# Performance work log

Measured on AMD Instinct MI355X. Metric: run time of the kernel, lower is better.

The kernel has to match this reference:

```python
import jax, jax.numpy as jnp
import numpy as np

N, M, D_MODEL, H, D_K, D_V = 2048, 2048, 1024, 16, 64, 64


def setup_inputs() -> dict:
    key = jax.random.key(0)
    ks = jax.random.split(key, 12)
    s = D_MODEL ** -0.5
    Q = jax.random.normal(ks[0], (N, D_MODEL), dtype=jnp.float32)
    K = jax.random.normal(ks[1], (M, D_MODEL), dtype=jnp.float32)
    V = jax.random.normal(ks[2], (M, D_MODEL), dtype=jnp.float32)
    mask = jnp.ones((N, M), dtype=bool)  # unused by the original forward
    # stacked per-head Linear params (torch Linear: y = x @ W.T + b); here stored as (H, in, out)
    Wq = jax.random.normal(ks[3], (H, D_MODEL, D_K), dtype=jnp.float32) * s
    bq = jax.random.normal(ks[4], (H, D_K), dtype=jnp.float32) * 0.01
    Wk = jax.random.normal(ks[5], (H, D_MODEL, D_K), dtype=jnp.float32) * s
    bk = jax.random.normal(ks[6], (H, D_K), dtype=jnp.float32) * 0.01
    Wv = jax.random.normal(ks[7], (H, D_MODEL, D_V), dtype=jnp.float32) * s
    bv = jax.random.normal(ks[8], (H, D_V), dtype=jnp.float32) * 0.01
    Wo = jax.random.normal(ks[9], (H * D_V, D_MODEL), dtype=jnp.float32) * ((H * D_V) ** -0.5)
    bo = jax.random.normal(ks[10], (D_MODEL,), dtype=jnp.float32) * 0.01
    return dict(Q=Q, K=K, V=V, mask=mask, Wq=Wq, bq=bq, Wk=Wk, bk=bk,
                Wv=Wv, bv=bv, Wo=Wo, bo=bo)


def reference(Q, K, V, mask, Wq, bq, Wk, bk, Wv, bv, Wo, bo):
    # per-head projections, batched over heads (h)
    Qh = jnp.einsum('nd,hdk->hnk', Q, Wq) + bq[:, None, :]  # (H, n, d_k)
    Kh = jnp.einsum('md,hdk->hmk', K, Wk) + bk[:, None, :]  # (H, m, d_k)
    Vh = jnp.einsum('md,hdv->hmv', V, Wv) + bv[:, None, :]  # (H, m, d_v)
    # faithful to source: scale d_k**-0.5 is applied AFTER the softmax
    scores = jnp.einsum('hnk,hmk->hnm', Qh, Kh)             # (H, n, m)
    attn = jax.nn.softmax(scores, axis=-1) * (D_K ** -0.5)
    heads = jnp.einsum('hnm,hmv->hnv', attn, Vh)            # (H, n, d_v)
    concat = jnp.transpose(heads, (1, 0, 2)).reshape(heads.shape[1], H * D_V)
    return concat @ Wo + bo                                  # (n, d_model)
```

## Files before the change

### kernel.cpp

```cpp
#include <hip/hip_runtime.h>

#define N_TOK 2048
#define DMODEL 1024
#define NH 16
#define DK 64
#define SOFF 48.0f

typedef __attribute__((ext_vector_type(8))) short bfrag;
typedef __attribute__((ext_vector_type(4))) float f32x4;
typedef __attribute__((ext_vector_type(16))) float f32x16;
typedef __attribute__((ext_vector_type(4))) unsigned u32x4;

__device__ __forceinline__ unsigned short f2bf(float f) {
    unsigned u = __builtin_bit_cast(unsigned, f);
    u += 0x7FFFu + ((u >> 16) & 1u);
    return (unsigned short)(u >> 16);
}
__device__ __forceinline__ float bf2f(unsigned short u) {
    unsigned x = ((unsigned)u) << 16;
    return __builtin_bit_cast(float, x);
}
__device__ __forceinline__ unsigned cvtpk(float lo, float hi) {
    unsigned r;
    asm volatile("v_cvt_pk_bf16_f32 %0, %1, %2" : "=v"(r) : "v"(lo), "v"(hi));
    return r;
}

__device__ __forceinline__ int swz(int row, int b) {
    return row * 128 + (b ^ ((row & 7) << 4));
}

__device__ __forceinline__ void gload16(const void* g, void* l) {
    __builtin_amdgcn_global_load_lds(
        (__attribute__((address_space(1))) void*)g,
        (__attribute__((address_space(3))) void*)l,
        16, 0, 0);
}

__global__ __launch_bounds__(256) void prep_kernel(
    const float* __restrict__ Qin, const float* __restrict__ Kin, const float* __restrict__ Vin,
    const float* __restrict__ Wq_, const float* __restrict__ Wk_, const float* __restrict__ Wv_,
    const float* __restrict__ Wo_,
    unsigned short* __restrict__ AhQ, unsigned short* __restrict__ AhK, unsigned short* __restrict__ AhV,
    unsigned short* __restrict__ WthQ, unsigned short* __restrict__ WthK, unsigned short* __restrict__ WthV,
    unsigned short* __restrict__ WoT)
{
    const int bid = blockIdx.x;
    const int tid = threadIdx.x;
    __shared__ float lds[64][65];

    if (bid < 3072) {
        const int z = bid >> 10, x = bid & 1023;
        const float* src = (z == 0) ? Qin : (z == 1) ? Kin : Vin;
        unsigned short* dh = (z == 0) ? AhQ : (z == 1) ? AhK : AhV;
        size_t base = ((size_t)x * 256 + tid) * 8;
        float4 a = *reinterpret_cast<const float4*>(src + base);
        float4 b = *reinterpret_cast<const float4*>(src + base + 4);
        float f[8] = {a.x, a.y, a.z, a.w, b.x, b.y, b.z, b.w};
        unsigned short hb[8];
        #pragma unroll
        for (int i = 0; i < 8; ++i) hb[i] = f2bf(f[i]);
        *reinterpret_cast<uint4*>(dh + base) = *reinterpret_cast<const uint4*>(hb);
    } else if (bid < 3840) {
        const int t = bid - 3072;
        const int z = t >> 8, rem = t & 255;
        const int h = rem >> 4, dt = rem & 15;
        const float* W = (z == 0) ? Wq_ : (z == 1) ? Wk_ : Wv_;
        unsigned short* oh = (z == 0) ? WthQ : (z == 1) ? WthK : WthV;

        {
            int rr = tid >> 2, c4 = (tid & 3) * 16;
            const float* src = W + ((size_t)h * DMODEL + dt * 64 + rr) * DK + c4;
            #pragma unroll
            for (int i = 0; i < 4; ++i) {
                float4 v = *reinterpret_cast<const float4*>(src + i * 4);
                lds[rr][c4 + i * 4 + 0] = v.x;
                lds[rr][c4 + i * 4 + 1] = v.y;
                lds[rr][c4 + i * 4 + 2] = v.z;
                lds[rr][c4 + i * 4 + 3] = v.w;
            }
        }
        __syncthreads();
        {
            int kk_ = tid >> 2, d4 = (tid & 3) * 16;
            unsigned short hb[16];
            #pragma unroll
            for (int i = 0; i < 16; ++i) hb[i] = f2bf(lds[d4 + i][kk_]);
            size_t o = (size_t)(h * 64 + kk_) * DMODEL + dt * 64 + d4;
            *reinterpret_cast<uint4*>(oh + o)     = *reinterpret_cast<const uint4*>(hb);
            *reinterpret_cast<uint4*>(oh + o + 8) = *reinterpret_cast<const uint4*>(hb + 8);
        }
    } else {
        const int t = bid - 3840;
        const int dt = t >> 4, jt = t & 15;
        {
            int rr = tid >> 2, c4 = (tid & 3) * 16;
            const float* src = Wo_ + (size_t)(dt * 64 + rr) * DMODEL + jt * 64 + c4;
            #pragma unroll
            for (int i = 0; i < 4; ++i) {
                float4 v = *reinterpret_cast<const float4*>(src + i * 4);
                lds[rr][c4 + i * 4 + 0] = v.x;
                lds[rr][c4 + i * 4 + 1] = v.y;
                lds[rr][c4 + i * 4 + 2] = v.z;
                lds[rr][c4 + i * 4 + 3] = v.w;
            }
        }
        __syncthreads();
        {
            int jj = tid >> 2, d4 = (tid & 3) * 16;
            unsigned short hb[16];
            #pragma unroll
            for (int i = 0; i < 16; ++i) hb[i] = f2bf(lds[d4 + i][jj]);
            size_t o = (size_t)(jt * 64 + jj) * DMODEL + dt * 64 + d4;
            *reinterpret_cast<uint4*>(WoT + o)     = *reinterpret_cast<const uint4*>(hb);
            *reinterpret_cast<uint4*>(WoT + o + 8) = *reinterpret_cast<const uint4*>(hb + 8);
        }
    }
}

__global__ __launch_bounds__(256) void proj_kernel(
    const unsigned short* __restrict__ AhQ, const unsigned short* __restrict__ AhK, const unsigned short* __restrict__ AhV,
    const unsigned short* __restrict__ WthQ, const unsigned short* __restrict__ WthK, const unsigned short* __restrict__ WthV,
    const float* __restrict__ bq_, const float* __restrict__ bk_, const float* __restrict__ bv_,
    unsigned short* __restrict__ Qhh,
    unsigned short* __restrict__ Khh,
    unsigned short* __restrict__ Vt)
{
    const int z = blockIdx.z;
    const unsigned short* Ah = (z == 0) ? AhK : (z == 1) ? AhQ : AhV;
    const unsigned short* Bh = (z == 0) ? WthK : (z == 1) ? WthQ : WthV;
    const float* bias = (z == 0) ? bk_ : (z == 1) ? bq_ : bv_;

    __shared__ alignas(16) unsigned char sAh[16384];
    __shared__ alignas(16) unsigned char sBh[16384];

    const int tid = threadIdx.x;
    const int lane = tid & 63;
    const int w = tid >> 6;
    const int wm = w >> 1, wn = w & 1;
    const int g = lane >> 4, li = lane & 15;

    const int row0 = blockIdx.x * 128;
    const int col0 = blockIdx.y * 128;

    f32x4 acc[4][4];
    #pragma unroll
    for (int m = 0; m < 4; ++m)
        #pragma unroll
        for (int n = 0; n < 4; ++n) acc[m][n] = f32x4{0.f, 0.f, 0.f, 0.f};

    for (int kt = 0; kt < DMODEL; kt += 64) {
        __syncthreads();
        #pragma unroll
        for (int p = 0; p < 4; ++p) {
            int chunk = p * 256 + tid;
            int r = chunk >> 3, cc = chunk & 7;
            int cs = (cc * 8) ^ ((r & 7) << 3);
            int ldso = (p * 256 + w * 64) * 16;
            gload16(Ah + (size_t)(row0 + r) * DMODEL + kt + cs, sAh + ldso);
            gload16(Bh + (size_t)(col0 + r) * DMODEL + kt + cs, sBh + ldso);
        }
        __syncthreads();

        #pragma unroll
        for (int kk = 0; kk < 2; ++kk) {
            bfrag afh[4], bfh[4];
            #pragma unroll
            for (int m = 0; m < 4; ++m)
                afh[m] = *reinterpret_cast<const bfrag*>(sAh + swz(wm * 64 + m * 16 + li, kk * 64 + g * 16));
            #pragma unroll
            for (int n = 0; n < 4; ++n)
                bfh[n] = *reinterpret_cast<const bfrag*>(sBh + swz(wn * 64 + n * 16 + li, kk * 64 + g * 16));
            #pragma unroll
            for (int m = 0; m < 4; ++m)
                #pragma unroll
                for (int n = 0; n < 4; ++n)
                    acc[m][n] = __builtin_amdgcn_mfma_f32_16x16x32_bf16(afh[m], bfh[n], acc[m][n], 0, 0, 0);
        }
    }

    #pragma unroll
    for (int m = 0; m < 4; ++m) {
        #pragma unroll
        for (int n = 0; n < 4; ++n) {
            int colg = col0 + wn * 64 + n * 16 + li;
            float bb = bias[colg];
            int hh = colg >> 6, k = colg & 63;
            int rowb = row0 + wm * 64 + m * 16 + g * 4;
            if (z == 2) {
                unsigned short vb4[4];
                #pragma unroll
                for (int r = 0; r < 4; ++r) vb4[r] = f2bf(acc[m][n][r] + bb);
                *reinterpret_cast<uint2*>(Vt + ((size_t)hh * DK + k) * N_TOK + rowb) =
                    *reinterpret_cast<const uint2*>(vb4);
            } else {
                #pragma unroll
                for (int r = 0; r < 4; ++r) {
                    size_t o = ((size_t)hh * N_TOK + rowb + r) * DK + k;
                    float val = acc[m][n][r] + bb;
                    if (z == 1) val *= 1.44269504088896f;
                    if (z == 0) Khh[o] = f2bf(val);
                    else        Qhh[o] = f2bf(val);
                }
            }
        }
    }
}

__global__ __launch_bounds__(256) void attn_kernel(
    const unsigned short* __restrict__ Qhh,
    const unsigned short* __restrict__ Khh,
    const unsigned short* __restrict__ Vt,
    unsigned short* __restrict__ Opart, float* __restrict__ lbuf)
{
    __shared__ alignas(16) unsigned char sKh[3][8192];
    __shared__ alignas(16) unsigned char sV [3][8192];

    const int bid = blockIdx.x;
    const int orig = (bid & 7) * 64 + (bid >> 3);
    const int h    = orig >> 5;
    const int half = (orig >> 4) & 1;
    const int qt   = orig & 15;

    const int tid  = threadIdx.x;
    const int lane = tid & 63;
    const int w    = tid >> 6;
    const int q31  = lane & 31;
    const int hi   = lane >> 5;
    const int qrow0 = qt * 128 + w * 32;

    const unsigned short* QbH = Qhh + (size_t)h * N_TOK * DK;
    const unsigned short* KbH = Khh + (size_t)h * N_TOK * DK;
    const unsigned short* Vtb = Vt  + (size_t)h * DK * N_TOK;

    bfrag bqh[4];
    #pragma unroll
    for (int d = 0; d < 4; ++d)
        bqh[d] = *reinterpret_cast<const bfrag*>(
            QbH + (size_t)(qrow0 + q31) * DK + d * 16 + hi * 8);

    f32x16 acc0 = {}, acc1 = {};
    float lrun = 0.f;

    const int tbase = half * (N_TOK / 2);

#define STAGE(B, T) do {                                                     \
    _Pragma("unroll")                                                        \
    for (int p_ = 0; p_ < 2; ++p_) {                                         \
        int chunk_ = p_ * 256 + w * 64 + lane;                               \
        int r_ = chunk_ >> 3;                                                \
        int cs_ = ((chunk_ & 7) * 8) ^ ((r_ & 7) << 3);                      \
        int ldso_ = (p_ * 256 + w * 64) * 16;                                \
        gload16(KbH + (size_t)((T) + r_) * DK + cs_, sKh[B] + ldso_);        \
        gload16(Vtb + (size_t)r_ * N_TOK + (T) + cs_, sV[B] + ldso_);        \
    } } while (0)

#define MKFRAG(W, PF) do {                                                   \
    _Pragma("unroll")                                                        \
    for (int kk_ = 0; kk_ < 2; ++kk_) {                                      \
        unsigned b0_ = W[4 * kk_ + 0], b1_ = W[4 * kk_ + 1];                 \
        unsigned a0_ = W[4 * kk_ + 2], a1_ = W[4 * kk_ + 3];                 \
        unsigned sb0_ = (unsigned)__shfl_xor((int)b0_, 32);                  \
        unsigned sa0_ = (unsigned)__shfl_xor((int)a0_, 32);                  \
        unsigned sb1_ = (unsigned)__shfl_xor((int)b1_, 32);                  \
        unsigned sa1_ = (unsigned)__shfl_xor((int)a1_, 32);                  \
        u32x4 t_ = { hi ? sa0_ : b0_, hi ? sa1_ : b1_,                       \
                     hi ? a0_ : sb0_, hi ? a1_ : sb1_ };                     \
        PF[kk_] = __builtin_bit_cast(bfrag, t_);                             \
    } } while (0)

    STAGE(0, tbase);

    int cur = 0;
    for (int tt = 0; tt < 16; ++tt) {
        int nxt = cur + 1; if (nxt == 3) nxt = 0;
        if (tt < 15) {
            STAGE(nxt, tbase + (tt + 1) * 64);
            asm volatile("s_waitcnt vmcnt(4)" ::: "memory");
        } else {
            asm volatile("s_waitcnt vmcnt(0)" ::: "memory");
        }
        __builtin_amdgcn_s_barrier();
        asm volatile("" ::: "memory");

        f32x16 s0, s1;
        #pragma unroll
        for (int r = 0; r < 16; ++r) { s0[r] = -SOFF; s1[r] = -SOFF; }
        __builtin_amdgcn_s_setprio(1);
        #pragma unroll
        for (int d = 0; d < 4; ++d) {
            const int bo = d * 32 + hi * 16;
            bfrag kh0 = *reinterpret_cast<const bfrag*>(sKh[cur] + swz(q31,      bo));
            bfrag kh1 = *reinterpret_cast<const bfrag*>(sKh[cur] + swz(32 + q31, bo));
            s0 = __builtin_amdgcn_mfma_f32_32x32x16_bf16(kh0, bqh[d], s0, 0, 0, 0);
            s1 = __builtin_amdgcn_mfma_f32_32x32x16_bf16(kh1, bqh[d], s1, 0, 0, 0);
        }
        __builtin_amdgcn_s_setprio(0);

        float p0[16], p1[16];
        #pragma unroll
        for (int r = 0; r < 16; ++r) p0[r] = __builtin_exp2f(s0[r]);
        #pragma unroll
        for (int r = 0; r < 16; ++r) p1[r] = __builtin_exp2f(s1[r]);
        float ps = ((p0[0] + p0[1]) + (p0[2] + p0[3])) + ((p0[4] + p0[5]) + (p0[6] + p0[7]))
                 + ((p0[8] + p0[9]) + (p0[10] + p0[11])) + ((p0[12] + p0[13]) + (p0[14] + p0[15]))
                 + ((p1[0] + p1[1]) + (p1[2] + p1[3])) + ((p1[4] + p1[5]) + (p1[6] + p1[7]))
                 + ((p1[8] + p1[9]) + (p1[10] + p1[11])) + ((p1[12] + p1[13]) + (p1[14] + p1[15]));
        ps += __shfl_xor(ps, 32);
        lrun += ps;

        unsigned w0[8], w1[8];
        #pragma unroll
        for (int j = 0; j < 8; ++j) w0[j] = cvtpk(p0[2 * j], p0[2 * j + 1]);
        #pragma unroll
        for (int j = 0; j < 8; ++j) w1[j] = cvtpk(p1[2 * j], p1[2 * j + 1]);
        bfrag pf0[2], pf1[2];
        MKFRAG(w0, pf0);
        MKFRAG(w1, pf1);

        __builtin_amdgcn_s_setprio(1);
        #pragma unroll
        for (int ks = 0; ks < 4; ++ks) {
            bfrag pb = (ks < 2) ? pf0[ks & 1] : pf1[ks & 1];
            const int bo = ks * 32 + hi * 16;
            bfrag va0 = *reinterpret_cast<const bfrag*>(sV[cur] + swz(q31,      bo));
            bfrag va1 = *reinterpret_cast<const bfrag*>(sV[cur] + swz(32 + q31, bo));
            acc0 = __builtin_amdgcn_mfma_f32_32x32x16_bf16(va0, pb, acc0, 0, 0, 0);
            acc1 = __builtin_amdgcn_mfma_f32_32x32x16_bf16(va1, pb, acc1, 0, 0, 0);
        }
        __builtin_amdgcn_s_setprio(0);
        asm volatile("" ::: "memory");
        cur = nxt;
    }
#undef STAGE
#undef MKFRAG

    const size_t idxp = (size_t)half * NH * N_TOK + (size_t)h * N_TOK + qrow0 + q31;
    unsigned short* op = Opart + idxp * 64;
    #pragma unroll
    for (int m = 0; m < 4; ++m) {
        uint2 wa = make_uint2(cvtpk(acc0[4 * m], acc0[4 * m + 1]),
                              cvtpk(acc0[4 * m + 2], acc0[4 * m + 3]));
        uint2 wb = make_uint2(cvtpk(acc1[4 * m], acc1[4 * m + 1]),
                              cvtpk(acc1[4 * m + 2], acc1[4 * m + 3]));
        *reinterpret_cast<uint2*>(op + 8 * m + 4 * hi)      = wa;
        *reinterpret_cast<uint2*>(op + 32 + 8 * m + 4 * hi) = wb;
    }
    if (lane < 32)
        lbuf[idxp] = lrun;
}

__global__ __launch_bounds__(256) void combine_kernel(
    const unsigned short* __restrict__ Opart, const float* __restrict__ lbuf,
    unsigned short* __restrict__ Hc)
{
    const int tid = threadIdx.x;
    const int sub = tid & 3;
    const int idx = blockIdx.x * 64 + (tid >> 2);
    const int h = idx >> 11, row = idx & 2047;
    const int HS = NH * N_TOK;

    float inv = 0.125f / (lbuf[idx] + lbuf[HS + idx]);

    const unsigned short* O1 = Opart + (size_t)idx * 64 + sub * 16;
    const unsigned short* O2 = Opart + ((size_t)HS + idx) * 64 + sub * 16;
    uint4 x1 = *reinterpret_cast<const uint4*>(O1);
    uint4 y1 = *reinterpret_cast<const uint4*>(O1 + 8);
    uint4 x2 = *reinterpret_cast<const uint4*>(O2);
    uint4 y2 = *reinterpret_cast<const uint4*>(O2 + 8);
    unsigned wa[8] = {x1.x, x1.y, x1.z, x1.w, y1.x, y1.y, y1.z, y1.w};
    unsigned wb[8] = {x2.x, x2.y, x2.z, x2.w, y2.x, y2.y, y2.z, y2.w};
    unsigned short hb[16];
    #pragma unroll
    for (int j = 0; j < 8; ++j) {
        float lo = (bf2f((unsigned short)(wa[j] & 0xFFFF)) +
                    bf2f((unsigned short)(wb[j] & 0xFFFF))) * inv;
        float hi2 = (bf2f((unsigned short)(wa[j] >> 16)) +
                     bf2f((unsigned short)(wb[j] >> 16))) * inv;
        hb[2 * j]     = f2bf(lo);
        hb[2 * j + 1] = f2bf(hi2);
    }
    size_t o = (size_t)row * DMODEL + h * 64 + sub * 16;
    *reinterpret_cast<uint4*>(Hc + o)     = *reinterpret_cast<const uint4*>(hb);
    *reinterpret_cast<uint4*>(Hc + o + 8) = *reinterpret_cast<const uint4*>(hb + 8);
}

__global__ __launch_bounds__(256) void oproj_kernel(
    const unsigned short* __restrict__ Hc,
    const unsigned short* __restrict__ WoT,
    const float* __restrict__ bo,
    float* __restrict__ out)
{
    __shared__ alignas(16) unsigned char sA[8192];
    __shared__ alignas(16) unsigned char sB[16384];

    const int tid = threadIdx.x;
    const int lane = tid & 63;
    const int w = tid >> 6;
    const int wm = w >> 1, wn = w & 1;
    const int g = lane >> 4, li = lane & 15;
    const int row0 = blockIdx.x * 64;
    const int col0 = blockIdx.y * 128;

    f32x4 acc[2][4];
    #pragma unroll
    for (int m = 0; m < 2; ++m)
        #pragma unroll
        for (int n = 0; n < 4; ++n) acc[m][n] = f32x4{0.f, 0.f, 0.f, 0.f};

    for (int kt = 0; kt < DMODEL; kt += 64) {
        __syncthreads();
        #pragma unroll
        for (int p = 0; p < 2; ++p) {
            int chunk = p * 256 + tid;
            int r = chunk >> 3, cc = chunk & 7;
            int cs = (cc * 8) ^ ((r & 7) << 3);
            int ldso = (p * 256 + w * 64) * 16;
            gload16(Hc + (size_t)(row0 + r) * DMODEL + kt + cs, sA + ldso);
        }
        #pragma unroll
        for (int p = 0; p < 4; ++p) {
            int chunk = p * 256 + tid;
            int r = chunk >> 3, cc = chunk & 7;
            int cs = (cc * 8) ^ ((r & 7) << 3);
            int ldso = (p * 256 + w * 64) * 16;
            gload16(WoT + (size_t)(col0 + r) * DMODEL + kt + cs, sB + ldso);
        }
        __syncthreads();

        #pragma unroll
        for (int kk = 0; kk < 2; ++kk) {
            bfrag af[2], bf_[4];
            #pragma unroll
            for (int m = 0; m < 2; ++m)
                af[m] = *reinterpret_cast<const bfrag*>(sA + swz(wm * 32 + m * 16 + li, kk * 64 + g * 16));
            #pragma unroll
            for (int n = 0; n < 4; ++n)
                bf_[n] = *reinterpret_cast<const bfrag*>(sB + swz(wn * 64 + n * 16 + li, kk * 64 + g * 16));
            #pragma unroll
            for (int m = 0; m < 2; ++m)
                #pragma unroll
                for (int n = 0; n < 4; ++n)
                    acc[m][n] = __builtin_amdgcn_mfma_f32_16x16x32_bf16(af[m], bf_[n], acc[m][n], 0, 0, 0);
        }
    }

    #pragma unroll
    for (int m = 0; m < 2; ++m) {
        #pragma unroll
        for (int n = 0; n < 4; ++n) {
            int colg = col0 + wn * 64 + n * 16 + li;
            float bb = bo[colg];
            #pragma unroll
            for (int r = 0; r < 4; ++r) {
                int rowg = row0 + wm * 32 + m * 16 + g * 4 + r;
                out[(size_t)rowg * DMODEL + colg] = acc[m][n][r] + bb;
            }
        }
    }
}

extern "C" void kernel_launch(void* const* d_in, const int* in_sizes, int n_in,
                              void* d_out, int out_size, void* d_ws, size_t ws_size,
                              hipStream_t stream) {
    (void)in_sizes; (void)n_in; (void)out_size; (void)ws_size;
    const float* Q  = (const float*)d_in[0];
    const float* K  = (const float*)d_in[1];
    const float* V  = (const float*)d_in[2];
    const float* Wq = (const float*)d_in[4];
    const float* bq = (const float*)d_in[5];
    const float* Wk = (const float*)d_in[6];
    const float* bk = (const float*)d_in[7];
    const float* Wv = (const float*)d_in[8];
    const float* bv = (const float*)d_in[9];
    const float* Wo = (const float*)d_in[10];
    const float* bo = (const float*)d_in[11];
    float* out = (float*)d_out;

    const size_t ASZ = (size_t)N_TOK * DMODEL;
    const size_t WSZ = (size_t)NH * DK * DMODEL;
    const size_t HSZ = (size_t)NH * N_TOK * DK;
    unsigned short* p = (unsigned short*)d_ws;
    unsigned short* AhQ = p; p += ASZ;
    unsigned short* AhK = p; p += ASZ;
    unsigned short* AhV = p; p += ASZ;
    unsigned short* WthQ = p; p += WSZ;
    unsigned short* WthK = p; p += WSZ;
    unsigned short* WthV = p; p += WSZ;
    unsigned short* Qhh = p; p += HSZ;
    unsigned short* Khh = p; p += HSZ;
    unsigned short* Vt  = p; p += HSZ;
    unsigned short* Hc  = p; p += HSZ;
    unsigned short* WoT = p; p += ASZ / 2;

    unsigned short* Opart = (unsigned short*)d_ws;
    float* lbuf = (float*)(Opart + (size_t)2 * NH * N_TOK * 64);

    prep_kernel<<<dim3(4096), 256, 0, stream>>>(
        Q, K, V, Wq, Wk, Wv, Wo,
        AhQ, AhK, AhV, WthQ, WthK, WthV, WoT);
    proj_kernel<<<dim3(16, 8, 3), 256, 0, stream>>>(
        AhQ, AhK, AhV, WthQ, WthK, WthV,
        bq, bk, bv, Qhh, Khh, Vt);
    attn_kernel<<<dim3(512), 256, 0, stream>>>(Qhh, Khh, Vt, Opart, lbuf);
    combine_kernel<<<dim3(512), 256, 0, stream>>>(Opart, lbuf, Hc);
    oproj_kernel<<<dim3(32, 8), 256, 0, stream>>>(Hc, WoT, bo, out);
}
```

Baseline: 95.00 us.

## Fuse split-softmax combine into output projection A-tile loads

Removes the separate combine kernel and the Hc intermediate buffer. The output projection now loads both partial attention outputs directly from Opart, normalizes them with per-row inverse sums precomputed into shared memory, converts to bf16 and stores the result into the A tile. This saves a kernel launch and a write plus re-read of the concatenated heads. In exchange, each column block reads twice as much A data and redoes the combine arithmetic. The asynchronous direct-to-LDS loads for the A tile are also replaced by register round-trip loads.

```diff
diff --git a/kernel.cpp b/kernel.cpp
--- a/kernel.cpp
+++ b/kernel.cpp
@@ -350,49 +350,15 @@
         lbuf[idxp] = lrun;
 }
 
-__global__ __launch_bounds__(256) void combine_kernel(
+__global__ __launch_bounds__(256) void oproj_kernel(
     const unsigned short* __restrict__ Opart, const float* __restrict__ lbuf,
-    unsigned short* __restrict__ Hc)
-{
-    const int tid = threadIdx.x;
-    const int sub = tid & 3;
-    const int idx = blockIdx.x * 64 + (tid >> 2);
-    const int h = idx >> 11, row = idx & 2047;
-    const int HS = NH * N_TOK;
-
-    float inv = 0.125f / (lbuf[idx] + lbuf[HS + idx]);
-
-    const unsigned short* O1 = Opart + (size_t)idx * 64 + sub * 16;
-    const unsigned short* O2 = Opart + ((size_t)HS + idx) * 64 + sub * 16;
-    uint4 x1 = *reinterpret_cast<const uint4*>(O1);
-    uint4 y1 = *reinterpret_cast<const uint4*>(O1 + 8);
-    uint4 x2 = *reinterpret_cast<const uint4*>(O2);
-    uint4 y2 = *reinterpret_cast<const uint4*>(O2 + 8);
-    unsigned wa[8] = {x1.x, x1.y, x1.z, x1.w, y1.x, y1.y, y1.z, y1.w};
-    unsigned wb[8] = {x2.x, x2.y, x2.z, x2.w, y2.x, y2.y, y2.z, y2.w};
-    unsigned short hb[16];
-    #pragma unroll
-    for (int j = 0; j < 8; ++j) {
-        float lo = (bf2f((unsigned short)(wa[j] & 0xFFFF)) +
-                    bf2f((unsigned short)(wb[j] & 0xFFFF))) * inv;
-        float hi2 = (bf2f((unsigned short)(wa[j] >> 16)) +
-                     bf2f((unsigned short)(wb[j] >> 16))) * inv;
-        hb[2 * j]     = f2bf(lo);
-        hb[2 * j + 1] = f2bf(hi2);
-    }
-    size_t o = (size_t)row * DMODEL + h * 64 + sub * 16;
-    *reinterpret_cast<uint4*>(Hc + o)     = *reinterpret_cast<const uint4*>(hb);
-    *reinterpret_cast<uint4*>(Hc + o + 8) = *reinterpret_cast<const uint4*>(hb + 8);
-}
-
-__global__ __launch_bounds__(256) void oproj_kernel(
-    const unsigned short* __restrict__ Hc,
     const unsigned short* __restrict__ WoT,
     const float* __restrict__ bo,
     float* __restrict__ out)
 {
     __shared__ alignas(16) unsigned char sA[8192];
     __shared__ alignas(16) unsigned char sB[16384];
+    __shared__ float sInv[NH][64];
 
     const int tid = threadIdx.x;
     const int lane = tid & 63;
@@ -401,6 +367,13 @@
     const int g = lane >> 4, li = lane & 15;
     const int row0 = blockIdx.x * 64;
     const int col0 = blockIdx.y * 128;
+    const int HS = NH * N_TOK;
+
+    for (int i = tid; i < NH * 64; i += 256) {
+        int hh = i >> 6, r = i & 63;
+        int idx = hh * N_TOK + row0 + r;
+        sInv[hh][r] = 0.125f / (lbuf[idx] + lbuf[HS + idx]);
+    }
 
     f32x4 acc[2][4];
     #pragma unroll
@@ -409,14 +382,29 @@
         for (int n = 0; n < 4; ++n) acc[m][n] = f32x4{0.f, 0.f, 0.f, 0.f};
 
     for (int kt = 0; kt < DMODEL; kt += 64) {
+        const int hh = kt >> 6;
         __syncthreads();
         #pragma unroll
         for (int p = 0; p < 2; ++p) {
             int chunk = p * 256 + tid;
             int r = chunk >> 3, cc = chunk & 7;
             int cs = (cc * 8) ^ ((r & 7) << 3);
-            int ldso = (p * 256 + w * 64) * 16;
-            gload16(Hc + (size_t)(row0 + r) * DMODEL + kt + cs, sA + ldso);
+            size_t idxp = (size_t)hh * N_TOK + row0 + r;
+            uint4 x1 = *reinterpret_cast<const uint4*>(Opart + idxp * 64 + cs);
+            uint4 x2 = *reinterpret_cast<const uint4*>(Opart + ((size_t)HS + idxp) * 64 + cs);
+            float inv = sInv[hh][r];
+            unsigned wa_[4] = {x1.x, x1.y, x1.z, x1.w};
+            unsigned wb_[4] = {x2.x, x2.y, x2.z, x2.w};
+            unsigned ow[4];
+            #pragma unroll
+            for (int j = 0; j < 4; ++j) {
+                float lo  = (bf2f((unsigned short)(wa_[j] & 0xFFFF)) +
+                             bf2f((unsigned short)(wb_[j] & 0xFFFF))) * inv;
+                float hi2 = (bf2f((unsigned short)(wa_[j] >> 16)) +
+                             bf2f((unsigned short)(wb_[j] >> 16))) * inv;
+                ow[j] = cvtpk(lo, hi2);
+            }
+            *reinterpret_cast<uint4*>(sA + chunk * 16) = *reinterpret_cast<const uint4*>(ow);
         }
         #pragma unroll
         for (int p = 0; p < 4; ++p) {
@@ -490,7 +478,6 @@
     unsigned short* Qhh = p; p += HSZ;
     unsigned short* Khh = p; p += HSZ;
     unsigned short* Vt  = p; p += HSZ;
-    unsigned short* Hc  = p; p += HSZ;
     unsigned short* WoT = p; p += ASZ / 2;
 
     unsigned short* Opart = (unsigned short*)d_ws;
@@ -503,6 +490,5 @@
         AhQ, AhK, AhV, WthQ, WthK, WthV,
         bq, bk, bv, Qhh, Khh, Vt);
     attn_kernel<<<dim3(512), 256, 0, stream>>>(Qhh, Khh, Vt, Opart, lbuf);
-    combine_kernel<<<dim3(512), 256, 0, stream>>>(Opart, lbuf, Hc);
-    oproj_kernel<<<dim3(32, 8), 256, 0, stream>>>(Hc, WoT, bo, out);
-}
+    oproj_kernel<<<dim3(32, 8), 256, 0, stream>>>(Opart, lbuf, WoT, bo, out);
+}
```

Measured after the change: 103.1 us. +8.5%, slower.
